# Kernel optimization log

Hardware: AMD Instinct MI355X
Metric: run time of the kernel (lower is better)

The kernel has to match this reference:

```python
import jax, jax.numpy as jnp
import numpy as np

B, N, D = 4, 512, 64
EPS = 1e-5          # nn.LayerNorm default
NEG_SLOPE = 0.01    # nn.LeakyReLU default


def setup_inputs() -> dict:
    key = jax.random.key(0)
    k1, k2, k3 = jax.random.split(key, 3)
    i_em = jax.random.normal(k1, (B, N, D), dtype=jnp.float32)
    # att_a: Linear(2*D -> 1); store weight as flat (2*D,) plus scalar bias
    W_a = jax.random.normal(k2, (2 * D,), dtype=jnp.float32) * 0.05
    b_a = jax.random.normal(k3, (1,), dtype=jnp.float32) * 0.05
    gamma = jnp.ones((D,), dtype=jnp.float32)
    beta = jnp.zeros((D,), dtype=jnp.float32)
    return {"i_em": i_em, "W_a": W_a, "b_a": b_a, "gamma": gamma, "beta": beta}


def reference(i_em, W_a, b_a, gamma, beta):
    # LayerNorm over last dim
    mu = jnp.mean(i_em, axis=-1, keepdims=True)
    var = jnp.mean(jnp.square(i_em - mu), axis=-1, keepdims=True)
    xn = (i_em - mu) * jax.lax.rsqrt(var + EPS) * gamma + beta  # [B,N,D]

    # Fused additive attention: cat(q,k) @ W == q @ W[:D] + k @ W[D:]
    a_q, a_k = W_a[:D], W_a[D:]
    sq = jnp.einsum("bnd,d->bn", xn, a_q)          # query contribution
    sk = jnp.einsum("bnd,d->bn", xn, a_k)          # key contribution
    scores = sq[:, :, None] + sk[:, None, :] + b_a[0]  # [B,N,N]
    scores = jnp.where(scores >= 0, scores, NEG_SLOPE * scores)  # LeakyReLU
    # dropout is identity in eval mode
    alphas = jax.nn.softmax(scores, axis=-1)[..., None]  # [B,N,N,1]

    # elementwise outer product on the UN-normalized embeddings
    value = i_em[:, :, None, :] * i_em[:, None, :, :]  # [B,N,N,D]
    return (alphas, value)
```

## Files before the change

kernel.cpp:

```cpp
#include <hip/hip_runtime.h>
#include <math.h>

#define BB 4
#define NN 512
#define DD 64
#define EPS 1e-5f
#define NEG_SLOPE 0.01f
#define TI 4

typedef float f32x4 __attribute__((ext_vector_type(4)));

__global__ void __launch_bounds__(256)
stats_kernel(const float* __restrict__ i_em,
             const float* __restrict__ W_a,
             const float* __restrict__ gamma,
             const float* __restrict__ beta,
             float* __restrict__ sq,
             float* __restrict__ sk) {
    int row  = (blockIdx.x * blockDim.x + threadIdx.x) >> 6;
    int lane = threadIdx.x & 63;
    if (row >= BB * NN) return;

    float x = i_em[row * DD + lane];

    float s = x;
    #pragma unroll
    for (int off = 32; off >= 1; off >>= 1) s += __shfl_xor(s, off, 64);
    float mu = s * (1.0f / DD);

    float dx = x - mu;
    float v = dx * dx;
    #pragma unroll
    for (int off = 32; off >= 1; off >>= 1) v += __shfl_xor(v, off, 64);
    float rstd = rsqrtf(v * (1.0f / DD) + EPS);

    float xn = dx * rstd * gamma[lane] + beta[lane];
    float pq = xn * W_a[lane];
    float pk = xn * W_a[DD + lane];
    #pragma unroll
    for (int off = 32; off >= 1; off >>= 1) {
        pq += __shfl_xor(pq, off, 64);
        pk += __shfl_xor(pk, off, 64);
    }
    if (lane == 0) { sq[row] = pq; sk[row] = pk; }
}

__global__ void __launch_bounds__(256)
attn_kernel(const float* __restrict__ i_em,
            const float* __restrict__ sq,
            const float* __restrict__ sk,
            const float* __restrict__ b_a,
            float* __restrict__ alphas,
            float* __restrict__ value) {
    const int blk  = blockIdx.x;
    const int i0g  = blk * TI;
    const int b    = i0g >> 9;
    const int t    = threadIdx.x;
    const int lane = t & 63;
    const int w    = t >> 6;

    const float bias = b_a[0];

    {
        const int row  = i0g + w;
        const float si = sq[row] + bias;
        const float* skb = sk + b * NN;

        float e[8];
        float m = -INFINITY;
        #pragma unroll
        for (int k = 0; k < 8; ++k) {
            float s = si + skb[lane + k * 64];
            s = (s >= 0.f) ? s : NEG_SLOPE * s;
            e[k] = s;
            m = fmaxf(m, s);
        }
        #pragma unroll
        for (int off = 32; off >= 1; off >>= 1) m = fmaxf(m, __shfl_xor(m, off, 64));

        float sum = 0.f;
        #pragma unroll
        for (int k = 0; k < 8; ++k) { e[k] = expf(e[k] - m); sum += e[k]; }
        #pragma unroll
        for (int off = 32; off >= 1; off >>= 1) sum += __shfl_xor(sum, off, 64);
        const float inv = 1.0f / sum;

        float* arow = alphas + (size_t)row * NN;
        #pragma unroll
        for (int k = 0; k < 8; ++k)
            __builtin_nontemporal_store(e[k] * inv, &arow[lane + k * 64]);
    }

    const f32x4* em4 = (const f32x4*)i_em;
    const int d4 = t & 15;
    const int jg = t >> 4;
    const f32x4* emb = em4 + (size_t)b * NN * 16;

    f32x4 xi[TI];
    #pragma unroll
    for (int r = 0; r < TI; ++r) xi[r] = em4[(size_t)(i0g + r) * 16 + d4];

    f32x4* out0 = (f32x4*)value + (size_t)i0g * (NN * 16) + d4;

    #pragma unroll 4
    for (int k = 0; k < NN / 16; ++k) {
        const int j = jg + k * 16;
        const f32x4 xj = emb[j * 16 + d4];
        #pragma unroll
        for (int r = 0; r < TI; ++r) {
            f32x4 o = xi[r] * xj;
            __builtin_nontemporal_store(o, out0 + (size_t)r * (NN * 16) + j * 16);
        }
    }
}

extern "C" void kernel_launch(void* const* d_in, const int* in_sizes, int n_in,
                              void* d_out, int out_size, void* d_ws, size_t ws_size,
                              hipStream_t stream) {
    const float* i_em  = (const float*)d_in[0];
    const float* W_a   = (const float*)d_in[1];
    const float* b_a   = (const float*)d_in[2];
    const float* gamma = (const float*)d_in[3];
    const float* beta  = (const float*)d_in[4];

    float* alphas = (float*)d_out;
    float* value  = (float*)d_out + (size_t)BB * NN * NN;

    float* sq = (float*)d_ws;
    float* sk = sq + BB * NN;

    stats_kernel<<<(BB * NN) / 4, 256, 0, stream>>>(i_em, W_a, gamma, beta, sq, sk);
    attn_kernel<<<(BB * NN) / TI, 256, 0, stream>>>(i_em, sq, sk, b_a, alphas, value);
}
```

Measured before the change: 281.8 us.

## Split attention kernel over 2D grid with j-chunks and larger row tile

Result: slower. 288.3 us (+2.3%).

```diff
diff --git a/kernel.cpp b/kernel.cpp
--- a/kernel.cpp
+++ b/kernel.cpp
@@ -6,7 +6,8 @@
 #define DD 64
 #define EPS 1e-5f
 #define NEG_SLOPE 0.01f
-#define TI 4
+#define TI 8
+#define JC 8
 
 typedef float f32x4 __attribute__((ext_vector_type(4)));
 
@@ -45,55 +46,64 @@
     if (lane == 0) { sq[row] = pq; sk[row] = pk; }
 }
 
-__global__ void __launch_bounds__(256)
+__global__ void __launch_bounds__(256, 8)
 attn_kernel(const float* __restrict__ i_em,
             const float* __restrict__ sq,
             const float* __restrict__ sk,
             const float* __restrict__ b_a,
             float* __restrict__ alphas,
             float* __restrict__ value) {
-    const int blk  = blockIdx.x;
-    const int i0g  = blk * TI;
+    const int ib   = blockIdx.x;
+    const int jc   = blockIdx.y;
+    const int i0g  = ib * TI;
     const int b    = i0g >> 9;
     const int t    = threadIdx.x;
     const int lane = t & 63;
     const int w    = t >> 6;
 
-    const float bias = b_a[0];
-
-    {
-        const int row  = i0g + w;
-        const float si = sq[row] + bias;
+    if (jc == 0) {
+        const float bias = b_a[0];
         const float* skb = sk + b * NN;
 
-        float e[8];
-        float m = -INFINITY;
+        float sv[8];
         #pragma unroll
-        for (int k = 0; k < 8; ++k) {
-            float s = si + skb[lane + k * 64];
-            s = (s >= 0.f) ? s : NEG_SLOPE * s;
-            e[k] = s;
-            m = fmaxf(m, s);
+        for (int k = 0; k < 8; ++k) sv[k] = skb[lane + k * 64];
+
+        #pragma unroll
+        for (int rr = 0; rr < 2; ++rr) {
+            const int row  = i0g + w + rr * 4;
+            const float si = sq[row] + bias;
+
+            float e[8];
+            float m = -INFINITY;
+            #pragma unroll
+            for (int k = 0; k < 8; ++k) {
+                float s = si + sv[k];
+                s = (s >= 0.f) ? s : NEG_SLOPE * s;
+                e[k] = s;
+                m = fmaxf(m, s);
+            }
+            #pragma unroll
+            for (int off = 32; off >= 1; off >>= 1) m = fmaxf(m, __shfl_xor(m, off, 64));
+
+            float sum = 0.f;
+            #pragma unroll
+            for (int k = 0; k < 8; ++k) { e[k] = expf(e[k] - m); sum += e[k]; }
+            #pragma unroll
+            for (int off = 32; off >= 1; off >>= 1) sum += __shfl_xor(sum, off, 64);
+            const float inv = 1.0f / sum;
+
+            float* arow = alphas + (size_t)row * NN;
+            #pragma unroll
+            for (int k = 0; k < 8; ++k)
+                __builtin_nontemporal_store(e[k] * inv, &arow[lane + k * 64]);
         }
-        #pragma unroll
-        for (int off = 32; off >= 1; off >>= 1) m = fmaxf(m, __shfl_xor(m, off, 64));
-
-        float sum = 0.f;
-        #pragma unroll
-        for (int k = 0; k < 8; ++k) { e[k] = expf(e[k] - m); sum += e[k]; }
-        #pragma unroll
-        for (int off = 32; off >= 1; off >>= 1) sum += __shfl_xor(sum, off, 64);
-        const float inv = 1.0f / sum;
-
-        float* arow = alphas + (size_t)row * NN;
-        #pragma unroll
-        for (int k = 0; k < 8; ++k)
-            __builtin_nontemporal_store(e[k] * inv, &arow[lane + k * 64]);
     }
 
     const f32x4* em4 = (const f32x4*)i_em;
     const int d4 = t & 15;
     const int jg = t >> 4;
+    const int j0 = jc * (NN / JC);
     const f32x4* emb = em4 + (size_t)b * NN * 16;
 
     f32x4 xi[TI];
@@ -102,9 +112,9 @@
 
     f32x4* out0 = (f32x4*)value + (size_t)i0g * (NN * 16) + d4;
 
-    #pragma unroll 4
-    for (int k = 0; k < NN / 16; ++k) {
-        const int j = jg + k * 16;
+    #pragma unroll
+    for (int k = 0; k < NN / JC / 16; ++k) {
+        const int j = j0 + jg + k * 16;
         const f32x4 xj = emb[j * 16 + d4];
         #pragma unroll
         for (int r = 0; r < TI; ++r) {
@@ -130,5 +140,6 @@
     float* sk = sq + BB * NN;
 
     stats_kernel<<<(BB * NN) / 4, 256, 0, stream>>>(i_em, W_a, gamma, beta, sq, sk);
-    attn_kernel<<<(BB * NN) / TI, 256, 0, stream>>>(i_em, sq, sk, b_a, alphas, value);
+    dim3 grid((BB * NN) / TI, JC);
+    attn_kernel<<<grid, 256, 0, stream>>>(i_em, sq, sk, b_a, alphas, value);
 }
```
